# Kernel tuning notes

Hardware: AMD Instinct MI355X
Metric: run time of the kernel (lower is better)

The kernel has to match this reference:

```python
import jax, jax.numpy as jnp
import numpy as np

N, E, H, HEADS, L, B = 16000, 256000, 192, 4, 4, 8
C = H // HEADS
VN, VE, T = 32, 8, 1000


def _sin_emb(t, dim):
    half = dim // 2
    freqs = jnp.exp(-np.log(10000.0) * jnp.arange(half, dtype=jnp.float32) / half)
    ang = t.astype(jnp.float32)[:, None] * freqs[None, :]
    return jnp.concatenate([jnp.sin(ang), jnp.cos(ang)], axis=-1)


def _ln(x, g, b, eps=1e-5):
    mu = jnp.mean(x, -1, keepdims=True)
    var = jnp.mean(jnp.square(x - mu), -1, keepdims=True)
    return (x - mu) * jax.lax.rsqrt(var + eps) * g + b


def setup_inputs():
    key = jax.random.key(0)
    ks = iter(jax.random.split(key, 64))
    p = lambda shape, s=0.02: jax.random.normal(next(ks), shape, jnp.float32) * s
    inp = {}
    inp['node_emb'] = p((VN, H))
    inp['edge_emb'] = p((VE, H))
    inp['time_w1'] = p((H, H)); inp['time_b1'] = jnp.zeros((H,), jnp.float32)
    inp['time_w2'] = p((H, H)); inp['time_b2'] = jnp.zeros((H,), jnp.float32)
    inp['mask_emb'] = p((2, H))
    inp['wq'] = p((L, H, H)); inp['bq'] = jnp.zeros((L, H), jnp.float32)
    inp['wk'] = p((L, H, H)); inp['bk'] = jnp.zeros((L, H), jnp.float32)
    inp['wv'] = p((L, H, H)); inp['bv'] = jnp.zeros((L, H), jnp.float32)
    inp['we'] = p((L, H, H))
    inp['wskip'] = p((L, H, H)); inp['bskip'] = jnp.zeros((L, H), jnp.float32)
    inp['wbeta'] = p((L, 3 * H))
    inp['ln_g'] = jnp.ones((L, H), jnp.float32); inp['ln_b'] = jnp.zeros((L, H), jnp.float32)
    inp['node_out_w'] = p((H, VN)); inp['node_out_b'] = jnp.zeros((VN,), jnp.float32)
    inp['edge_w1'] = p((4 * H, H)); inp['edge_b1'] = jnp.zeros((H,), jnp.float32)
    inp['edge_w2'] = p((H, VE)); inp['edge_b2'] = jnp.zeros((VE,), jnp.float32)
    inp['node_type'] = jax.random.randint(next(ks), (N,), 0, VN)
    inp['edge_type'] = jax.random.randint(next(ks), (E,), 0, VE)
    inp['edge_index'] = jax.random.randint(next(ks), (2, E), 0, N)
    inp['edit_mask'] = jax.random.randint(next(ks), (N,), 0, 2, dtype=jnp.int32)
    inp['node_batch'] = jnp.sort(jax.random.randint(next(ks), (N,), 0, B))
    inp['t_graph'] = jax.random.randint(next(ks), (B,), 1, T)
    return inp


def reference(node_emb, edge_emb, time_w1, time_b1, time_w2, time_b2, mask_emb,
              wq, bq, wk, bk, wv, bv, we, wskip, bskip, wbeta, ln_g, ln_b,
              node_out_w, node_out_b, edge_w1, edge_b1, edge_w2, edge_b2,
              node_type, edge_type, edge_index, edit_mask, node_batch, t_graph):
    src, dst = edge_index[0], edge_index[1]
    # time embedding: sinusoidal -> Linear -> SiLU -> Linear  => [B, H]
    t_vec = jax.nn.silu(_sin_emb(t_graph, H) @ time_w1 + time_b1) @ time_w2 + time_b2
    t_node = t_vec[node_batch]              # [N, H]
    t_edge = t_vec[node_batch[src]]         # [E, H]
    x = node_emb[node_type] + t_node + mask_emb[edit_mask]
    edge_attr = edge_emb[edge_type] + t_edge
    scale = 1.0 / np.sqrt(C)
    for l in range(L):
        q = (x @ wq[l] + bq[l]).reshape(N, HEADS, C)
        k = (x @ wk[l] + bk[l]).reshape(N, HEADS, C)
        v = (x @ wv[l] + bv[l]).reshape(N, HEADS, C)
        e = (edge_attr @ we[l]).reshape(E, HEADS, C)
        kj = k[src] + e                                   # [E, heads, C]
        score = jnp.sum(q[dst] * kj, axis=-1) * scale      # [E, heads]
        m = jax.ops.segment_max(score, dst, num_segments=N)
        ex = jnp.exp(score - m[dst])
        denom = jax.ops.segment_sum(ex, dst, num_segments=N)
        alpha = ex / denom[dst]
        msg = (v[src] + e) * alpha[..., None]              # [E, heads, C]
        out = jax.ops.segment_sum(msg, dst, num_segments=N).reshape(N, H)
        xr = x @ wskip[l] + bskip[l]
        beta = jax.nn.sigmoid(jnp.concatenate([out, xr, out - xr], -1) @ wbeta[l])[:, None]
        h = beta * xr + (1.0 - beta) * out
        x = _ln(x + h, ln_g[l], ln_b[l])
    node_logits = x @ node_out_w + node_out_b
    edge_feat = jnp.concatenate([x[src], x[dst], edge_attr, t_edge], -1)  # [E, 4H]
    edge_logits = jax.nn.silu(edge_feat @ edge_w1 + edge_b1) @ edge_w2 + edge_b2
    return node_logits, edge_logits
```

## Files before the change

### kernel.cpp

```cpp
#include <hip/hip_runtime.h>
#include <hip/hip_bf16.h>
#include <math.h>

#define NN 16000
#define NPAD 16128
#define NE 256000
#define H 192
#define RP 256
#define KVR 512
#define NL 4
#define NBATCH 8
#define VEt 8
#define HH (H*H)
#define EML 16

typedef __hip_bfloat16 bf16;
typedef unsigned short u16;
typedef unsigned char u8;
typedef unsigned int u32;
typedef __attribute__((ext_vector_type(8))) short bfrag_t;
typedef __attribute__((ext_vector_type(4))) float facc_t;
typedef __attribute__((ext_vector_type(4))) float f4;
typedef __attribute__((ext_vector_type(2))) unsigned int u32x2;

__device__ __forceinline__ bf16 f2b(float v){ return __float2bfloat16(v); }
__device__ __forceinline__ int rfl(int v){ return __builtin_amdgcn_readfirstlane(v); }

__device__ __forceinline__ unsigned enc8sw(float x){
    unsigned u = __float_as_uint(x);
    unsigned s = (u >> 24) & 0x80u;
    float ax = fabsf(x);
    if(ax >= 448.f) return s | 0x7Eu;
    if(ax < 0.015625f){
        int q = (int)rintf(ax * 512.f);
        return s | (unsigned)q;
    }
    unsigned au = u & 0x7FFFFFFFu;
    unsigned lsb = (au >> 20) & 1u;
    au += 0x7FFFFu + lsb;
    unsigned E = (au >> 23) - 127u;
    unsigned M = (au >> 20) & 7u;
    if((int)E > 8) return s | 0x7Eu;
    return s | ((E + 7u) << 3) | M;
}
__device__ __forceinline__ unsigned enc8(float x){
#if __has_builtin(__builtin_amdgcn_cvt_pk_fp8_f32)
    return (u32)__builtin_amdgcn_cvt_pk_fp8_f32(x, x, 0, false) & 0xFFu;
#else
    return enc8sw(x);
#endif
}
template<int SEL>
__device__ __forceinline__ float dec8s(u32 w){
#if __has_builtin(__builtin_amdgcn_cvt_f32_fp8)
    return __builtin_amdgcn_cvt_f32_fp8((int)w, SEL);
#else
    unsigned v = (w >> (SEL*8)) & 0xFFu;
    unsigned e = (v >> 3) & 15u, m = v & 7u;
    float mag = e ? __builtin_ldexpf((float)(8u + m), (int)e - 10)
                  : __builtin_ldexpf((float)m, -9);
    return (v & 0x80u) ? -mag : mag;
#endif
}
__device__ __forceinline__ float frcp(float x){
#if __has_builtin(__builtin_amdgcn_rcpf)
    return __builtin_amdgcn_rcpf(x);
#else
    return 1.f/x;
#endif
}

__global__ void k_sentinel(float* __restrict__ out, float v){ out[0] = v; }

__global__ void k_transpose(const float* __restrict__ wq, const float* __restrict__ wk,
                            const float* __restrict__ wv, const float* __restrict__ wsk,
                            const float* __restrict__ w1, const float* __restrict__ now,
                            const float* __restrict__ ew2, u16* __restrict__ wt){
    int mat = blockIdx.x;
    if(mat < 18){
        const float* src;
        if(mat < 4)       src = wq  + (size_t)mat*HH;
        else if(mat < 8)  src = wk  + (size_t)(mat-4)*HH;
        else if(mat < 12) src = wv  + (size_t)(mat-8)*HH;
        else if(mat < 16) src = wsk + (size_t)(mat-12)*HH;
        else              src = w1  + (size_t)(mat-16)*HH;
        u16* dst = wt + (size_t)mat*HH;
        const int slice = HH/8;
        int base = blockIdx.y*slice;
        for(int i = base + threadIdx.x; i < base + slice; i += blockDim.x){
            int k = i / H, n = i % H;
            bf16 b = f2b(src[i]);
            dst[n*H + k] = *(u16*)&b;
        }
    } else if(mat == 18){
        u16* dst = wt + (size_t)18*HH;
        const int slice = (32*192)/8;
        int base = blockIdx.y*slice;
        for(int i = base + threadIdx.x; i < base + slice; i += blockDim.x){
            int k = i >> 5, n = i & 31;
            bf16 b = f2b(now[i]);
            dst[n*192 + k] = *(u16*)&b;
        }
    } else {
        u16* dst = wt + (size_t)18*HH + 32*192;
        const int slice = (16*192)/8;
        int base = blockIdx.y*slice;
        for(int i = base + threadIdx.x; i < base + slice; i += blockDim.x){
            int k = i >> 4, n = i & 15;
            float v = (n < 8) ? ew2[k*8 + n] : 0.f;
            bf16 b = f2b(v);
            dst[n*192 + k] = *(u16*)&b;
        }
    }
}

__global__ void k_tvec(const int* __restrict__ tg, const float* __restrict__ w1,
                       const float* __restrict__ b1, const float* __restrict__ w2,
                       const float* __restrict__ b2, float* __restrict__ tvec){
    int b = blockIdx.x, j = threadIdx.x;
    __shared__ float emb[H], h1[H];
    float t = (float)tg[b];
    if(j < 96){
        float fr = __expf(-logf(10000.0f) * (float)j / 96.0f);
        float ang = t * fr;
        emb[j]      = sinf(ang);
        emb[j + 96] = cosf(ang);
    }
    __syncthreads();
    float acc = b1[j];
    for(int k = 0; k < H; k++) acc += emb[k] * w1[k*H + j];
    h1[j] = acc / (1.f + __expf(-acc));
    __syncthreads();
    float acc2 = b2[j];
    for(int k = 0; k < H; k++) acc2 += h1[k] * w2[k*H + j];
    tvec[b*H + j] = acc2;
}

__global__ void k_init_x(const float* __restrict__ nemb, const float* __restrict__ memb,
                         const float* __restrict__ tvec, const int* __restrict__ ntype,
                         const int* __restrict__ emask, const int* __restrict__ nbatch,
                         float* __restrict__ x, u16* __restrict__ xb){
    int idx = blockIdx.x*blockDim.x + threadIdx.x;
    if(idx >= NN*H) return;
    int n = idx / H, c = idx % H;
    float v = nemb[(size_t)ntype[n]*H + c] + tvec[nbatch[n]*H + c]
            + memb[(size_t)emask[n]*H + c];
    x[idx] = v;
    bf16 b = f2b(v); xb[idx] = *(u16*)&b;
}

__global__ void k_zero_i(int* __restrict__ p, int n){
    int i = blockIdx.x*blockDim.x + threadIdx.x;
    if(i < n) p[i] = 0;
}
__global__ void k_count(const int* __restrict__ edst, int* __restrict__ cnt){
    int e = blockIdx.x*blockDim.x + threadIdx.x;
    if(e < NE) atomicAdd(&cnt[edst[e]], 1);
}
__global__ __launch_bounds__(1024) void k_scan(const int* __restrict__ cnt,
                                               int* __restrict__ ofs, int* __restrict__ cur){
    __shared__ int wsum[16];
    __shared__ int carry_s;
    int tid = threadIdx.x, lane = tid & 63, w = tid >> 6;
    if(tid == 0) carry_s = 0;
    __syncthreads();
    for(int base = 0; base < NN; base += 1024){
        int idx = base + tid;
        int v = (idx < NN) ? cnt[idx] : 0;
        int sc = v;
        #pragma unroll
        for(int o = 1; o < 64; o <<= 1){
            int t = __shfl_up(sc, o);
            if(lane >= o) sc += t;
        }
        if(lane == 63) wsum[w] = sc;
        __syncthreads();
        if(w == 0){
            int ws = (lane < 16) ? wsum[lane] : 0;
            #pragma unroll
            for(int o = 1; o < 16; o <<= 1){
                int t = __shfl_up(ws, o);
                if(lane >= o) ws += t;
            }
            if(lane < 16) wsum[lane] = ws;
        }
        __syncthreads();
        int wbase = (w > 0) ? wsum[w-1] : 0;
        int c = carry_s;
        int excl = c + wbase + sc - v;
        if(idx < NN){ ofs[idx] = excl; cur[idx] = excl; }
        __syncthreads();
        if(tid == 0) carry_s = c + wsum[15];
        __syncthreads();
    }
    if(threadIdx.x == 0) ofs[NN] = carry_s;
}
__global__ void k_scatter(const int* __restrict__ esrc, const int* __restrict__ edst,
                          const int* __restrict__ etype, const int* __restrict__ nbatch,
                          int* __restrict__ cur, int2* __restrict__ spair){
    int e = blockIdx.x*blockDim.x + threadIdx.x;
    if(e >= NE) return;
    int s = esrc[e], d = edst[e];
    int pos = atomicAdd(&cur[d], 1);
    int2 se; se.x = s*KVR; se.y = (nbatch[s]*VEt + etype[e])*KVR;
    spair[pos] = se;
}

__global__ void k_tabs(const float* __restrict__ eemb, const float* __restrict__ tvec,
                       const float* __restrict__ we,
                       const float* __restrict__ w1, const float* __restrict__ b1,
                       u16* __restrict__ etab, u16* __restrict__ ctab){
    int blk = blockIdx.x;
    int c = threadIdx.x;
    __shared__ float a[H];
    if(blk < NL*64){
        int l = blk >> 6, idx = blk & 63, b = idx >> 3, et = idx & 7;
        a[c] = eemb[et*H + c] + tvec[b*H + c];
        __syncthreads();
        float acc = 0.f;
        const float* w = we + (size_t)l*HH;
        for(int k = 0; k < H; k++) acc += a[k] * w[k*H + c];
        bf16 bv = f2b(acc);
        etab[(size_t)blk*256 + (c/3)*4 + (c%3)] = *(u16*)&bv;
    } else {
        int idx = blk - NL*64, b = idx >> 3, et = idx & 7;
        a[c] = eemb[et*H + c] + tvec[b*H + c];
        __syncthreads();
        float acc = b1[c];
        for(int k = 0; k < H; k++){
            acc += a[k]          * w1[(size_t)(2*H + k)*H + c];
            acc += tvec[b*H + k] * w1[(size_t)(3*H + k)*H + c];
        }
        bf16 bv = f2b(acc);
        ctab[(size_t)idx*256 + (c/3)*4 + (c%3)] = *(u16*)&bv;
    }
}

struct GemmP {
    const u16* wt[4];
    const float* bias[4];
    void* out[4];
    int obf[4];
};
__global__ __launch_bounds__(256) void k_gemm(const u16* __restrict__ A, GemmP P){
    int oi = blockIdx.y / 3, nt = blockIdx.y % 3;
    const u16* Wt = P.wt[oi];
    const float* bias = P.bias[oi];
    int wave = rfl(threadIdx.x >> 6), lane = threadIdx.x & 63;
    int quad = lane >> 4, l16 = lane & 15;
    int m0 = blockIdx.x*256 + wave*64;
    int n0 = nt*64;
    facc_t acc[4][4];
    #pragma unroll
    for(int i = 0; i < 4; i++)
        #pragma unroll
        for(int j = 0; j < 4; j++){ acc[i][j][0]=0.f; acc[i][j][1]=0.f; acc[i][j][2]=0.f; acc[i][j][3]=0.f; }
    #pragma unroll
    for(int kc = 0; kc < 6; kc++){
        int kb = kc*32 + quad*8;
        bfrag_t af[4], bg[4];
        #pragma unroll
        for(int i = 0; i < 4; i++) af[i] = *(const bfrag_t*)(A  + (size_t)(m0 + i*16 + l16)*H + kb);
        #pragma unroll
        for(int j = 0; j < 4; j++) bg[j] = *(const bfrag_t*)(Wt + (size_t)(n0 + j*16 + l16)*H + kb);
        #pragma unroll
        for(int i = 0; i < 4; i++)
            #pragma unroll
            for(int j = 0; j < 4; j++)
                acc[i][j] = __builtin_amdgcn_mfma_f32_16x16x32_bf16(af[i], bg[j], acc[i][j], 0, 0, 0);
    }
    float bv[4];
    #pragma unroll
    for(int j = 0; j < 4; j++) bv[j] = bias ? bias[n0 + j*16 + l16] : 0.f;
    int mode = P.obf[oi];
    if(mode != 0){
        u8* out = (u8*)P.out[oi];
        int rstride = (mode == 2) ? RP : KVR;
        int mult    = (mode == 2) ? 4  : 8;
        int koff    = (mode == 4) ? 4  : 0;
        int byteoff[4];
        #pragma unroll
        for(int j = 0; j < 4; j++){
            int c = n0 + j*16 + l16;
            byteoff[j] = (c/3)*mult + (c%3) + koff;
        }
        #pragma unroll
        for(int i = 0; i < 4; i++){
            int rb = m0 + i*16 + quad*4;
            #pragma unroll
            for(int r = 0; r < 4; r++){
                int row = rb + r;
                if(row < NN){
                    #pragma unroll
                    for(int j = 0; j < 4; j++)
                        out[(size_t)row*rstride + byteoff[j]] = (u8)enc8(acc[i][j][r] + bv[j]);
                }
            }
        }
    } else {
        float* out = (float*)P.out[oi];
        #pragma unroll
        for(int i = 0; i < 4; i++){
            int rb = m0 + i*16 + quad*4;
            #pragma unroll
            for(int r = 0; r < 4; r++){
                int row = rb + r;
                if(row < NN){
                    #pragma unroll
                    for(int j = 0; j < 4; j++)
                        out[(size_t)row*H + n0 + j*16 + l16] = acc[i][j][r] + bv[j];
                }
            }
        }
    }
}

__global__ __launch_bounds__(256) void k_attn(
    const float* __restrict__ Q, const u8* __restrict__ KVb,
    const float* __restrict__ XR,
    const u16* __restrict__ etab, const int* __restrict__ ofs,
    const int2* __restrict__ spair,
    const float* __restrict__ wb, const float* __restrict__ lng, const float* __restrict__ lnb,
    float* __restrict__ x, u16* __restrict__ xb)
{
    int wv = rfl(threadIdx.x >> 6);
    int n = blockIdx.x*4 + wv;
    int lane = threadIdx.x & 63;
    int lane8 = lane*8;
    int ch = lane*3;
    size_t base = (size_t)n*H + ch;
    const float scale = 0.14433756729740646f;
    float q0 = Q[base], q1 = Q[base+1], q2 = Q[base+2];
    int p0 = ofs[n], p1 = ofs[n+1];
    float lac[4]  = {0.f,0.f,0.f,0.f};
    float ac0[4]  = {0.f,0.f,0.f,0.f};
    float ac1[4]  = {0.f,0.f,0.f,0.f};
    float ac2[4]  = {0.f,0.f,0.f,0.f};
    const u8* etb = (const u8*)etab;
    int p = p0;
    u32x2 kvc[4], ewc[4];
    bool have = (p + 3 < p1);
    if(have){
        #pragma unroll
        for(int t = 0; t < 4; t++){
            int2 se = spair[p+t];
            kvc[t] = *(const u32x2*)(KVb + se.x + lane8);
            ewc[t] = *(const u32x2*)(etb + se.y + lane8);
        }
    }
    while(have){
        int pn = p + 4;
        bool more = (pn + 3 < p1);
        u32x2 kvn[4], ewn[4];
        if(more){
            #pragma unroll
            for(int t = 0; t < 4; t++){
                int2 se = spair[pn+t];
                kvn[t] = *(const u32x2*)(KVb + se.x + lane8);
                ewn[t] = *(const u32x2*)(etb + se.y + lane8);
            }
        }
        float e0[4], e1[4], e2[4], tt[4];
        #pragma unroll
        for(int t = 0; t < 4; t++){
            e0[t] = __uint_as_float(ewc[t].x << 16);
            e1[t] = __uint_as_float(ewc[t].x & 0xffff0000u);
            e2[t] = __uint_as_float(ewc[t].y << 16);
            tt[t] = q0*(dec8s<0>(kvc[t].x)+e0[t]) + q1*(dec8s<1>(kvc[t].x)+e1[t])
                  + q2*(dec8s<2>(kvc[t].x)+e2[t]);
        }
        #pragma unroll
        for(int o = 1; o <= 8; o <<= 1){
            #pragma unroll
            for(int t = 0; t < 4; t++) tt[t] += __shfl_xor(tt[t], o);
        }
        #pragma unroll
        for(int t = 0; t < 4; t++){
            float sc = fminf(fmaxf(tt[t]*scale, -60.f), 60.f);
            float pw = __expf(sc);
            lac[t] += pw;
            ac0[t] += pw*(dec8s<0>(kvc[t].y)+e0[t]);
            ac1[t] += pw*(dec8s<1>(kvc[t].y)+e1[t]);
            ac2[t] += pw*(dec8s<2>(kvc[t].y)+e2[t]);
        }
        if(more){
            #pragma unroll
            for(int t = 0; t < 4; t++){ kvc[t] = kvn[t]; ewc[t] = ewn[t]; }
        }
        p = pn;
        have = more;
    }
    for(; p < p1; p++){
        int soA = spair[p].x, eoA = spair[p].y;
        u32x2 kvA = *(const u32x2*)(KVb + soA + lane8);
        u32x2 ewA = *(const u32x2*)(etb + eoA + lane8);
        float e0A = __uint_as_float(ewA.x << 16);
        float e1A = __uint_as_float(ewA.x & 0xffff0000u);
        float e2A = __uint_as_float(ewA.y << 16);
        float tA = q0*(dec8s<0>(kvA.x)+e0A) + q1*(dec8s<1>(kvA.x)+e1A) + q2*(dec8s<2>(kvA.x)+e2A);
        tA += __shfl_xor(tA,1); tA += __shfl_xor(tA,2); tA += __shfl_xor(tA,4); tA += __shfl_xor(tA,8);
        float sc = fminf(fmaxf(tA*scale, -60.f), 60.f);
        float pw = __expf(sc);
        lac[0] += pw;
        ac0[0] += pw*(dec8s<0>(kvA.y)+e0A);
        ac1[0] += pw*(dec8s<1>(kvA.y)+e1A);
        ac2[0] += pw*(dec8s<2>(kvA.y)+e2A);
    }
    float l  = (lac[0]+lac[1]) + (lac[2]+lac[3]);
    float a0 = (ac0[0]+ac0[1]) + (ac0[2]+ac0[3]);
    float a1 = (ac1[0]+ac1[1]) + (ac1[2]+ac1[3]);
    float a2 = (ac2[0]+ac2[1]) + (ac2[2]+ac2[3]);
    float inv = (p1 > p0) ? 1.f/l : 0.f;
    float o0 = a0*inv, o1 = a1*inv, o2 = a2*inv;
    float xr0 = XR[base], xr1 = XR[base+1], xr2 = XR[base+2];
    float sd = o0*wb[ch]  + o1*wb[ch+1]  + o2*wb[ch+2]
             + xr0*wb[H+ch] + xr1*wb[H+ch+1] + xr2*wb[H+ch+2]
             + (o0-xr0)*wb[2*H+ch] + (o1-xr1)*wb[2*H+ch+1] + (o2-xr2)*wb[2*H+ch+2];
    sd += __shfl_xor(sd,1); sd += __shfl_xor(sd,2); sd += __shfl_xor(sd,4);
    sd += __shfl_xor(sd,8); sd += __shfl_xor(sd,16); sd += __shfl_xor(sd,32);
    float beta = 1.f/(1.f + __expf(-sd));
    float h0 = beta*xr0 + (1.f-beta)*o0;
    float h1 = beta*xr1 + (1.f-beta)*o1;
    float h2 = beta*xr2 + (1.f-beta)*o2;
    float y0 = x[base] + h0, y1 = x[base+1] + h1, y2 = x[base+2] + h2;
    float s3 = y0 + y1 + y2;
    float q3 = y0*y0 + y1*y1 + y2*y2;
    #pragma unroll
    for(int o = 1; o <= 32; o <<= 1){
        s3 += __shfl_xor(s3, o);
        q3 += __shfl_xor(q3, o);
    }
    float mean = s3 * (1.f/H);
    float var = fmaxf(q3*(1.f/H) - mean*mean, 0.f);
    float rs = rsqrtf(var + 1e-5f);
    float d0 = y0-mean, d1 = y1-mean, d2 = y2-mean;
    float z0 = d0*rs*lng[ch]   + lnb[ch];
    float z1 = d1*rs*lng[ch+1] + lnb[ch+1];
    float z2 = d2*rs*lng[ch+2] + lnb[ch+2];
    x[base] = z0; x[base+1] = z1; x[base+2] = z2;
    bf16 t0 = f2b(z0), t1 = f2b(z1), t2 = f2b(z2);
    xb[base] = *(u16*)&t0; xb[base+1] = *(u16*)&t1; xb[base+2] = *(u16*)&t2;
}

__global__ __launch_bounds__(256) void k_nodeout(const u16* __restrict__ A, const u16* __restrict__ Wt,
                                                 const float* __restrict__ b, float* __restrict__ out){
    int wave = rfl(threadIdx.x >> 6), lane = threadIdx.x & 63;
    int quad = lane >> 4, l16 = lane & 15;
    int m0 = blockIdx.x*256 + wave*64;
    facc_t acc[4][2];
    #pragma unroll
    for(int i = 0; i < 4; i++)
        #pragma unroll
        for(int j = 0; j < 2; j++){ acc[i][j][0]=0.f; acc[i][j][1]=0.f; acc[i][j][2]=0.f; acc[i][j][3]=0.f; }
    #pragma unroll
    for(int kc = 0; kc < 6; kc++){
        int kb = kc*32 + quad*8;
        bfrag_t af[4], bg[2];
        #pragma unroll
        for(int i = 0; i < 4; i++) af[i] = *(const bfrag_t*)(A  + (size_t)(m0 + i*16 + l16)*H + kb);
        #pragma unroll
        for(int j = 0; j < 2; j++) bg[j] = *(const bfrag_t*)(Wt + (size_t)(j*16 + l16)*H + kb);
        #pragma unroll
        for(int i = 0; i < 4; i++)
            #pragma unroll
            for(int j = 0; j < 2; j++)
                acc[i][j] = __builtin_amdgcn_mfma_f32_16x16x32_bf16(af[i], bg[j], acc[i][j], 0, 0, 0);
    }
    float bv[2];
    #pragma unroll
    for(int j = 0; j < 2; j++) bv[j] = b[j*16 + l16];
    #pragma unroll
    for(int i = 0; i < 4; i++){
        int rb = m0 + i*16 + quad*4;
        #pragma unroll
        for(int r = 0; r < 4; r++){
            int row = rb + r;
            if(row < NN){
                #pragma unroll
                for(int j = 0; j < 2; j++)
                    out[(size_t)row*32 + j*16 + l16] = acc[i][j][r] + bv[j];
            }
        }
    }
}

__global__ __launch_bounds__(256) void k_edgemlp(
    const int* __restrict__ esrc, const int* __restrict__ edst, const int* __restrict__ etype,
    const int* __restrict__ nb,
    const u8* __restrict__ xs1, const u8* __restrict__ xd1, const u16* __restrict__ ctab,
    const u16* __restrict__ w2t, const float* __restrict__ b2p, float* __restrict__ out)
{
    __shared__ u16 hbuf[4][16][200];
    int wave = rfl(threadIdx.x >> 6);
    int lane = threadIdx.x & 63;
    int lane8 = lane*8;
    int l16 = lane & 15, quad = lane >> 4;
    int wid = blockIdx.x*4 + wave;
    int e0 = wid*EML;
    const u8* ctb = (const u8*)ctab;
    bfrag_t bg[6];
    #pragma unroll
    for(int kc = 0; kc < 6; kc++)
        bg[kc] = *(const bfrag_t*)(w2t + (size_t)l16*192 + kc*32 + quad*8);
    for(int eb = 0; eb < EML; eb += 2){
        int eX = e0 + eb, eY = e0 + eb + 1;
        int sX = esrc[eX], dX = edst[eX];
        int sY = esrc[eY], dY = edst[eY];
        int coX = (nb[sX]*VEt + etype[eX])*KVR;
        int coY = (nb[sY]*VEt + etype[eY])*KVR;
        u32 awX = *(const u32*)(xs1 + (size_t)sX*RP + lane*4);
        u32 awY = *(const u32*)(xs1 + (size_t)sY*RP + lane*4);
        u32 bwX = *(const u32*)(xd1 + (size_t)dX*RP + lane*4);
        u32 bwY = *(const u32*)(xd1 + (size_t)dY*RP + lane*4);
        u32x2 cwX = *(const u32x2*)(ctb + coX + lane8);
        u32x2 cwY = *(const u32x2*)(ctb + coY + lane8);
        float cfX0 = __uint_as_float(cwX.x << 16);
        float cfX1 = __uint_as_float(cwX.x & 0xffff0000u);
        float cfX2 = __uint_as_float(cwX.y << 16);
        float cfY0 = __uint_as_float(cwY.x << 16);
        float cfY1 = __uint_as_float(cwY.x & 0xffff0000u);
        float cfY2 = __uint_as_float(cwY.y << 16);
        float hX0, hX1, hX2, hY0, hY1, hY2;
        { float v = dec8s<0>(awX)+dec8s<0>(bwX)+cfX0; hX0 = v*frcp(1.f+__expf(-v)); }
        { float v = dec8s<1>(awX)+dec8s<1>(bwX)+cfX1; hX1 = v*frcp(1.f+__expf(-v)); }
        { float v = dec8s<2>(awX)+dec8s<2>(bwX)+cfX2; hX2 = v*frcp(1.f+__expf(-v)); }
        { float v = dec8s<0>(awY)+dec8s<0>(bwY)+cfY0; hY0 = v*frcp(1.f+__expf(-v)); }
        { float v = dec8s<1>(awY)+dec8s<1>(bwY)+cfY1; hY1 = v*frcp(1.f+__expf(-v)); }
        { float v = dec8s<2>(awY)+dec8s<2>(bwY)+cfY2; hY2 = v*frcp(1.f+__expf(-v)); }
        u16* rowX = &hbuf[wave][eb][0];
        u16* rowY = &hbuf[wave][eb+1][0];
        bf16 x0 = f2b(hX0), x1 = f2b(hX1), x2 = f2b(hX2);
        bf16 y0 = f2b(hY0), y1 = f2b(hY1), y2 = f2b(hY2);
        rowX[lane*3+0] = *(u16*)&x0; rowX[lane*3+1] = *(u16*)&x1; rowX[lane*3+2] = *(u16*)&x2;
        rowY[lane*3+0] = *(u16*)&y0; rowY[lane*3+1] = *(u16*)&y1; rowY[lane*3+2] = *(u16*)&y2;
    }
    __syncthreads();
    facc_t acc;
    acc[0]=0.f; acc[1]=0.f; acc[2]=0.f; acc[3]=0.f;
    #pragma unroll
    for(int kc = 0; kc < 6; kc++){
        bfrag_t af = *(const bfrag_t*)&hbuf[wave][l16][kc*32 + quad*8];
        acc = __builtin_amdgcn_mfma_f32_16x16x32_bf16(af, bg[kc], acc, 0, 0, 0);
    }
    if(l16 < 8){
        float bo = b2p[l16];
        #pragma unroll
        for(int r = 0; r < 4; r++){
            int e = e0 + quad*4 + r;
            out[(size_t)e*8 + l16] = acc[r] + bo;
        }
    }
}

extern "C" void kernel_launch(void* const* d_in, const int* in_sizes, int n_in,
                              void* d_out, int out_size, void* d_ws, size_t ws_size,
                              hipStream_t stream)
{
    {
        int bad = -1;
        if(n_in != 31) bad = 100;
        else {
            const int chk_idx[9] = {0, 7, 16, 21, 23, 26, 27, 29, 30};
            const int chk_sz [9] = {32*H, NL*HH, NL*3*H, 4*HH, H*8, NE, 2*NE, NN, NBATCH};
            for(int i = 0; i < 9; i++) if(in_sizes[chk_idx[i]] != chk_sz[i]){ bad = chk_idx[i]; break; }
        }
        if(bad >= 0){ k_sentinel<<<1,1,0,stream>>>((float*)d_out, 20000.f + 256.f*bad); return; }
        if(out_size != NN*32 + NE*8){ k_sentinel<<<1,1,0,stream>>>((float*)d_out, 30000.f); return; }
    }

    const float* node_emb = (const float*)d_in[0];
    const float* edge_emb = (const float*)d_in[1];
    const float* time_w1  = (const float*)d_in[2];
    const float* time_b1  = (const float*)d_in[3];
    const float* time_w2  = (const float*)d_in[4];
    const float* time_b2  = (const float*)d_in[5];
    const float* mask_emb = (const float*)d_in[6];
    const float* wq       = (const float*)d_in[7];
    const float* bq       = (const float*)d_in[8];
    const float* wk       = (const float*)d_in[9];
    const float* bk       = (const float*)d_in[10];
    const float* wv       = (const float*)d_in[11];
    const float* bv       = (const float*)d_in[12];
    const float* we       = (const float*)d_in[13];
    const float* wskip    = (const float*)d_in[14];
    const float* bskip    = (const float*)d_in[15];
    const float* wbeta    = (const float*)d_in[16];
    const float* ln_g     = (const float*)d_in[17];
    const float* ln_b     = (const float*)d_in[18];
    const float* now      = (const float*)d_in[19];
    const float* nob      = (const float*)d_in[20];
    const float* ew1      = (const float*)d_in[21];
    const float* eb1      = (const float*)d_in[22];
    const float* ew2      = (const float*)d_in[23];
    const float* eb2      = (const float*)d_in[24];
    const int* node_type  = (const int*)d_in[25];
    const int* edge_type  = (const int*)d_in[26];
    const int* edge_index = (const int*)d_in[27];
    const int* edit_mask  = (const int*)d_in[28];
    const int* node_batch = (const int*)d_in[29];
    const int* t_graph    = (const int*)d_in[30];
    const int* esrc = edge_index;
    const int* edst = edge_index + NE;

    char* wsb = (char*)d_ws;
    size_t off = 0;
    auto take = [&](size_t bytes) -> char* {
        char* r = wsb + off;
        off += (bytes + 255) & ~(size_t)255;
        return r;
    };
    float* tvec = (float*)take((size_t)NBATCH*H*4);
    float* x    = (float*)take((size_t)NN*H*4);
    u16*   xb   = (u16*)  take((size_t)NPAD*H*2);
    float* Q    = (float*)take((size_t)NN*H*4);
    u8*    KVb  = (u8*)   take((size_t)NN*KVR);
    float* XR   = (float*)take((size_t)NN*H*4);
    u8*    xs1  = (u8*)   take((size_t)NN*RP);
    u8*    xd1  = (u8*)   take((size_t)NN*RP);
    u16*   etab = (u16*)  take((size_t)NL*64*KVR);
    u16*   ctab = (u16*)  take((size_t)64*KVR);
    u16*   wt   = (u16*)  take((size_t)(18*HH + 32*192 + 16*192)*2);
    int* cnt    = (int*)  take((size_t)(NN+1)*4);
    int* offa   = (int*)  take((size_t)(NN+1)*4);
    int* cur    = (int*)  take((size_t)(NN+1)*4);
    int2* spair = (int2*) take((size_t)NE*8);

    if(ws_size < off){
        k_sentinel<<<1,1,0,stream>>>((float*)d_out, 10000.f + (float)(ws_size >> 20));
        return;
    }

    u16* w32t = wt + (size_t)18*HH;
    u16* w2t  = w32t + 32*192;

    k_transpose<<<dim3(20, 8), 256, 0, stream>>>(wq, wk, wv, wskip, ew1, now, ew2, wt);
    k_tvec<<<NBATCH, H, 0, stream>>>(t_graph, time_w1, time_b1, time_w2, time_b2, tvec);
    k_init_x<<<(NN*H + 255)/256, 256, 0, stream>>>(node_emb, mask_emb, tvec, node_type,
                                                   edit_mask, node_batch, x, xb);
    k_zero_i<<<(NN + 255)/256, 256, 0, stream>>>(cnt, NN);
    k_count<<<NE/256, 256, 0, stream>>>(edst, cnt);
    k_scan<<<1, 1024, 0, stream>>>(cnt, offa, cur);
    k_scatter<<<NE/256, 256, 0, stream>>>(esrc, edst, edge_type, node_batch, cur, spair);
    k_tabs<<<NL*64 + 64, H, 0, stream>>>(edge_emb, tvec, we, ew1, eb1, etab, ctab);

    for(int l = 0; l < NL; l++){
        GemmP P;
        P.wt[0] = wt + (size_t)(0  + l)*HH;  P.bias[0] = bq   + (size_t)l*H;  P.out[0] = Q;   P.obf[0] = 0;
        P.wt[1] = wt + (size_t)(4  + l)*HH;  P.bias[1] = bk   + (size_t)l*H;  P.out[1] = KVb; P.obf[1] = 3;
        P.wt[2] = wt + (size_t)(8  + l)*HH;  P.bias[2] = bv   + (size_t)l*H;  P.out[2] = KVb; P.obf[2] = 4;
        P.wt[3] = wt + (size_t)(12 + l)*HH;  P.bias[3] = bskip+ (size_t)l*H;  P.out[3] = XR;  P.obf[3] = 0;
        k_gemm<<<dim3(63, 12), 256, 0, stream>>>(xb, P);
        k_attn<<<NN/4, 256, 0, stream>>>(Q, KVb, XR, etab + (size_t)l*64*256, offa, spair,
                                         wbeta + (size_t)l*3*H, ln_g + (size_t)l*H,
                                         ln_b + (size_t)l*H, x, xb);
    }
    {
        GemmP P;
        P.wt[0] = wt + (size_t)16*HH; P.bias[0] = nullptr; P.out[0] = xs1; P.obf[0] = 2;
        P.wt[1] = wt + (size_t)17*HH; P.bias[1] = nullptr; P.out[1] = xd1; P.obf[1] = 2;
        P.wt[2] = P.wt[0]; P.bias[2] = nullptr; P.out[2] = xs1; P.obf[2] = 2;
        P.wt[3] = P.wt[0]; P.bias[3] = nullptr; P.out[3] = xs1; P.obf[3] = 2;
        k_gemm<<<dim3(63, 6), 256, 0, stream>>>(xb, P);
    }
    k_nodeout<<<63, 256, 0, stream>>>(xb, w32t, nob, (float*)d_out);
    k_edgemlp<<<NE/(4*EML), 256, 0, stream>>>(esrc, edst, edge_type, node_batch, xs1, xd1, ctab,
                                              w2t, eb2, (float*)d_out + (size_t)NN*32);
}
```

Baseline: 502.3 us.

## Fuse setup kernels, store Q as packed bf16, precompute edge indices, packed fp8 decode

Merges the weight transpose, time embedding and counter zeroing into one launch, and merges x init, degree counting and edge tables into another. This cuts the number of small kernel launches. Q is now written by the GEMM as bf16 in the padded attention layout, which roughly halves its read traffic in the attention kernel but lowers its precision. The scatter pass precomputes per-edge src, dst and table offsets so the edge MLP needs one int4 load instead of several dependent gathers. fp8 decode uses the packed two-value conversion where it is available.

```diff
diff --git a/kernel.cpp b/kernel.cpp
--- a/kernel.cpp
+++ b/kernel.cpp
@@ -22,6 +22,7 @@
 typedef __attribute__((ext_vector_type(4))) float facc_t;
 typedef __attribute__((ext_vector_type(4))) float f4;
 typedef __attribute__((ext_vector_type(2))) unsigned int u32x2;
+typedef __attribute__((ext_vector_type(2))) float f2v;
 
 __device__ __forceinline__ bf16 f2b(float v){ return __float2bfloat16(v); }
 __device__ __forceinline__ int rfl(int v){ return __builtin_amdgcn_readfirstlane(v); }
@@ -62,6 +63,13 @@
     return (v & 0x80u) ? -mag : mag;
 #endif
 }
+__device__ __forceinline__ f2v dec8pk01(u32 w){
+#if __has_builtin(__builtin_amdgcn_cvt_pk_f32_fp8)
+    return __builtin_amdgcn_cvt_pk_f32_fp8((int)w, false);
+#else
+    f2v r; r.x = dec8s<0>(w); r.y = dec8s<1>(w); return r;
+#endif
+}
 __device__ __forceinline__ float frcp(float x){
 #if __has_builtin(__builtin_amdgcn_rcpf)
     return __builtin_amdgcn_rcpf(x);
@@ -72,91 +80,131 @@
 
 __global__ void k_sentinel(float* __restrict__ out, float v){ out[0] = v; }
 
-__global__ void k_transpose(const float* __restrict__ wq, const float* __restrict__ wk,
-                            const float* __restrict__ wv, const float* __restrict__ wsk,
-                            const float* __restrict__ w1, const float* __restrict__ now,
-                            const float* __restrict__ ew2, u16* __restrict__ wt){
-    int mat = blockIdx.x;
-    if(mat < 18){
-        const float* src;
-        if(mat < 4)       src = wq  + (size_t)mat*HH;
-        else if(mat < 8)  src = wk  + (size_t)(mat-4)*HH;
-        else if(mat < 12) src = wv  + (size_t)(mat-8)*HH;
-        else if(mat < 16) src = wsk + (size_t)(mat-12)*HH;
-        else              src = w1  + (size_t)(mat-16)*HH;
-        u16* dst = wt + (size_t)mat*HH;
-        const int slice = HH/8;
-        int base = blockIdx.y*slice;
-        for(int i = base + threadIdx.x; i < base + slice; i += blockDim.x){
-            int k = i / H, n = i % H;
-            bf16 b = f2b(src[i]);
-            dst[n*H + k] = *(u16*)&b;
-        }
-    } else if(mat == 18){
-        u16* dst = wt + (size_t)18*HH;
-        const int slice = (32*192)/8;
-        int base = blockIdx.y*slice;
-        for(int i = base + threadIdx.x; i < base + slice; i += blockDim.x){
-            int k = i >> 5, n = i & 31;
-            bf16 b = f2b(now[i]);
-            dst[n*192 + k] = *(u16*)&b;
+__global__ void k_prep0(const float* __restrict__ wq, const float* __restrict__ wk,
+                        const float* __restrict__ wv, const float* __restrict__ wsk,
+                        const float* __restrict__ w1, const float* __restrict__ now,
+                        const float* __restrict__ ew2, u16* __restrict__ wt,
+                        const int* __restrict__ tg, const float* __restrict__ tw1,
+                        const float* __restrict__ tb1, const float* __restrict__ tw2,
+                        const float* __restrict__ tb2, float* __restrict__ tvec,
+                        int* __restrict__ cnt){
+    int blk = blockIdx.x;
+    if(blk < 160){
+        int mat = blk >> 3, ys = blk & 7;
+        if(mat < 18){
+            const float* src;
+            if(mat < 4)       src = wq  + (size_t)mat*HH;
+            else if(mat < 8)  src = wk  + (size_t)(mat-4)*HH;
+            else if(mat < 12) src = wv  + (size_t)(mat-8)*HH;
+            else if(mat < 16) src = wsk + (size_t)(mat-12)*HH;
+            else              src = w1  + (size_t)(mat-16)*HH;
+            u16* dst = wt + (size_t)mat*HH;
+            const int slice = HH/8;
+            int base = ys*slice;
+            for(int i = base + threadIdx.x; i < base + slice; i += blockDim.x){
+                int k = i / H, n = i % H;
+                bf16 b = f2b(src[i]);
+                dst[n*H + k] = *(u16*)&b;
+            }
+        } else if(mat == 18){
+            u16* dst = wt + (size_t)18*HH;
+            const int slice = (32*192)/8;
+            int base = ys*slice;
+            for(int i = base + threadIdx.x; i < base + slice; i += blockDim.x){
+                int k = i >> 5, n = i & 31;
+                bf16 b = f2b(now[i]);
+                dst[n*192 + k] = *(u16*)&b;
+            }
+        } else {
+            u16* dst = wt + (size_t)18*HH + 32*192;
+            const int slice = (16*192)/8;
+            int base = ys*slice;
+            for(int i = base + threadIdx.x; i < base + slice; i += blockDim.x){
+                int k = i >> 4, n = i & 15;
+                float v = (n < 8) ? ew2[k*8 + n] : 0.f;
+                bf16 b = f2b(v);
+                dst[n*192 + k] = *(u16*)&b;
+            }
+        }
+    } else if(blk < 168){
+        int b = blk - 160, j = threadIdx.x;
+        __shared__ float emb[H], h1[H];
+        float t = (float)tg[b];
+        if(j < 96){
+            float fr = __expf(-logf(10000.0f) * (float)j / 96.0f);
+            float ang = t * fr;
+            emb[j]      = sinf(ang);
+            emb[j + 96] = cosf(ang);
+        }
+        __syncthreads();
+        if(j < H){
+            float acc = tb1[j];
+            for(int k = 0; k < H; k++) acc += emb[k] * tw1[k*H + j];
+            h1[j] = acc / (1.f + __expf(-acc));
+        }
+        __syncthreads();
+        if(j < H){
+            float acc2 = tb2[j];
+            for(int k = 0; k < H; k++) acc2 += h1[k] * tw2[k*H + j];
+            tvec[b*H + j] = acc2;
         }
     } else {
-        u16* dst = wt + (size_t)18*HH + 32*192;
-        const int slice = (16*192)/8;
-        int base = blockIdx.y*slice;
-        for(int i = base + threadIdx.x; i < base + slice; i += blockDim.x){
-            int k = i >> 4, n = i & 15;
-            float v = (n < 8) ? ew2[k*8 + n] : 0.f;
-            bf16 b = f2b(v);
-            dst[n*192 + k] = *(u16*)&b;
-        }
-    }
-}
-
-__global__ void k_tvec(const int* __restrict__ tg, const float* __restrict__ w1,
-                       const float* __restrict__ b1, const float* __restrict__ w2,
-                       const float* __restrict__ b2, float* __restrict__ tvec){
-    int b = blockIdx.x, j = threadIdx.x;
-    __shared__ float emb[H], h1[H];
-    float t = (float)tg[b];
-    if(j < 96){
-        float fr = __expf(-logf(10000.0f) * (float)j / 96.0f);
-        float ang = t * fr;
-        emb[j]      = sinf(ang);
-        emb[j + 96] = cosf(ang);
-    }
-    __syncthreads();
-    float acc = b1[j];
-    for(int k = 0; k < H; k++) acc += emb[k] * w1[k*H + j];
-    h1[j] = acc / (1.f + __expf(-acc));
-    __syncthreads();
-    float acc2 = b2[j];
-    for(int k = 0; k < H; k++) acc2 += h1[k] * w2[k*H + j];
-    tvec[b*H + j] = acc2;
-}
-
-__global__ void k_init_x(const float* __restrict__ nemb, const float* __restrict__ memb,
-                         const float* __restrict__ tvec, const int* __restrict__ ntype,
-                         const int* __restrict__ emask, const int* __restrict__ nbatch,
-                         float* __restrict__ x, u16* __restrict__ xb){
-    int idx = blockIdx.x*blockDim.x + threadIdx.x;
-    if(idx >= NN*H) return;
-    int n = idx / H, c = idx % H;
-    float v = nemb[(size_t)ntype[n]*H + c] + tvec[nbatch[n]*H + c]
-            + memb[(size_t)emask[n]*H + c];
-    x[idx] = v;
-    bf16 b = f2b(v); xb[idx] = *(u16*)&b;
-}
-
-__global__ void k_zero_i(int* __restrict__ p, int n){
-    int i = blockIdx.x*blockDim.x + threadIdx.x;
-    if(i < n) p[i] = 0;
-}
-__global__ void k_count(const int* __restrict__ edst, int* __restrict__ cnt){
-    int e = blockIdx.x*blockDim.x + threadIdx.x;
-    if(e < NE) atomicAdd(&cnt[edst[e]], 1);
-}
+        int i = (blk - 168)*256 + threadIdx.x;
+        if(i < NN+1) cnt[i] = 0;
+    }
+}
+
+__global__ void k_prep1(const float* __restrict__ nemb, const float* __restrict__ memb,
+                        const float* __restrict__ tvec, const int* __restrict__ ntype,
+                        const int* __restrict__ emask, const int* __restrict__ nbatch,
+                        float* __restrict__ x, u16* __restrict__ xb,
+                        const int* __restrict__ edst, int* __restrict__ cnt,
+                        const float* __restrict__ eemb, const float* __restrict__ we,
+                        const float* __restrict__ w1, const float* __restrict__ b1,
+                        u16* __restrict__ etab, u16* __restrict__ ctab){
+    int blk = blockIdx.x;
+    if(blk < 12000){
+        int idx = blk*256 + threadIdx.x;
+        int n = idx / H, c = idx % H;
+        float v = nemb[(size_t)ntype[n]*H + c] + tvec[nbatch[n]*H + c]
+                + memb[(size_t)emask[n]*H + c];
+        x[idx] = v;
+        bf16 b = f2b(v); xb[idx] = *(u16*)&b;
+    } else if(blk < 13000){
+        int e = (blk - 12000)*256 + threadIdx.x;
+        atomicAdd(&cnt[edst[e]], 1);
+    } else {
+        int blk2 = blk - 13000;
+        int c = threadIdx.x;
+        __shared__ float a[H];
+        if(blk2 < NL*64){
+            int l = blk2 >> 6, idx = blk2 & 63, b = idx >> 3, et = idx & 7;
+            if(c < H) a[c] = eemb[et*H + c] + tvec[b*H + c];
+            __syncthreads();
+            if(c < H){
+                float acc = 0.f;
+                const float* w = we + (size_t)l*HH;
+                for(int k = 0; k < H; k++) acc += a[k] * w[k*H + c];
+                bf16 bv = f2b(acc);
+                etab[(size_t)blk2*256 + (c/3)*4 + (c%3)] = *(u16*)&bv;
+            }
+        } else {
+            int idx = blk2 - NL*64, b = idx >> 3, et = idx & 7;
+            if(c < H) a[c] = eemb[et*H + c] + tvec[b*H + c];
+            __syncthreads();
+            if(c < H){
+                float acc = b1[c];
+                for(int k = 0; k < H; k++){
+                    acc += a[k]          * w1[(size_t)(2*H + k)*H + c];
+                    acc += tvec[b*H + k] * w1[(size_t)(3*H + k)*H + c];
+                }
+                bf16 bv = f2b(acc);
+                ctab[(size_t)idx*256 + (c/3)*4 + (c%3)] = *(u16*)&bv;
+            }
+        }
+    }
+}
+
 __global__ __launch_bounds__(1024) void k_scan(const int* __restrict__ cnt,
                                                int* __restrict__ ofs, int* __restrict__ cur){
     __shared__ int wsum[16];
@@ -197,43 +245,15 @@
 }
 __global__ void k_scatter(const int* __restrict__ esrc, const int* __restrict__ edst,
                           const int* __restrict__ etype, const int* __restrict__ nbatch,
-                          int* __restrict__ cur, int2* __restrict__ spair){
+                          int* __restrict__ cur, int2* __restrict__ spair, int4* __restrict__ eprep){
     int e = blockIdx.x*blockDim.x + threadIdx.x;
     if(e >= NE) return;
     int s = esrc[e], d = edst[e];
+    int ct = (nbatch[s]*VEt + etype[e])*KVR;
     int pos = atomicAdd(&cur[d], 1);
-    int2 se; se.x = s*KVR; se.y = (nbatch[s]*VEt + etype[e])*KVR;
+    int2 se; se.x = s*KVR; se.y = ct;
     spair[pos] = se;
-}
-
-__global__ void k_tabs(const float* __restrict__ eemb, const float* __restrict__ tvec,
-                       const float* __restrict__ we,
-                       const float* __restrict__ w1, const float* __restrict__ b1,
-                       u16* __restrict__ etab, u16* __restrict__ ctab){
-    int blk = blockIdx.x;
-    int c = threadIdx.x;
-    __shared__ float a[H];
-    if(blk < NL*64){
-        int l = blk >> 6, idx = blk & 63, b = idx >> 3, et = idx & 7;
-        a[c] = eemb[et*H + c] + tvec[b*H + c];
-        __syncthreads();
-        float acc = 0.f;
-        const float* w = we + (size_t)l*HH;
-        for(int k = 0; k < H; k++) acc += a[k] * w[k*H + c];
-        bf16 bv = f2b(acc);
-        etab[(size_t)blk*256 + (c/3)*4 + (c%3)] = *(u16*)&bv;
-    } else {
-        int idx = blk - NL*64, b = idx >> 3, et = idx & 7;
-        a[c] = eemb[et*H + c] + tvec[b*H + c];
-        __syncthreads();
-        float acc = b1[c];
-        for(int k = 0; k < H; k++){
-            acc += a[k]          * w1[(size_t)(2*H + k)*H + c];
-            acc += tvec[b*H + k] * w1[(size_t)(3*H + k)*H + c];
-        }
-        bf16 bv = f2b(acc);
-        ctab[(size_t)idx*256 + (c/3)*4 + (c%3)] = *(u16*)&bv;
-    }
+    eprep[e] = make_int4(s*RP, d*RP, ct, 0);
 }
 
 struct GemmP {
@@ -273,7 +293,30 @@
     #pragma unroll
     for(int j = 0; j < 4; j++) bv[j] = bias ? bias[n0 + j*16 + l16] : 0.f;
     int mode = P.obf[oi];
-    if(mode != 0){
+    if(mode == 5){
+        u16* outp = (u16*)P.out[oi];
+        int hoff[4];
+        #pragma unroll
+        for(int j = 0; j < 4; j++){
+            int c = n0 + j*16 + l16;
+            hoff[j] = (c/3)*4 + (c%3);
+        }
+        #pragma unroll
+        for(int i = 0; i < 4; i++){
+            int rb = m0 + i*16 + quad*4;
+            #pragma unroll
+            for(int r = 0; r < 4; r++){
+                int row = rb + r;
+                if(row < NN){
+                    #pragma unroll
+                    for(int j = 0; j < 4; j++){
+                        bf16 b = f2b(acc[i][j][r] + bv[j]);
+                        outp[(size_t)row*256 + hoff[j]] = *(u16*)&b;
+                    }
+                }
+            }
+        }
+    } else if(mode != 0){
         u8* out = (u8*)P.out[oi];
         int rstride = (mode == 2) ? RP : KVR;
         int mult    = (mode == 2) ? 4  : 8;
@@ -316,7 +359,7 @@
 }
 
 __global__ __launch_bounds__(256) void k_attn(
-    const float* __restrict__ Q, const u8* __restrict__ KVb,
+    const u8* __restrict__ Qb, const u8* __restrict__ KVb,
     const float* __restrict__ XR,
     const u16* __restrict__ etab, const int* __restrict__ ofs,
     const int2* __restrict__ spair,
@@ -330,7 +373,10 @@
     int ch = lane*3;
     size_t base = (size_t)n*H + ch;
     const float scale = 0.14433756729740646f;
-    float q0 = Q[base], q1 = Q[base+1], q2 = Q[base+2];
+    u32x2 qw = *(const u32x2*)(Qb + (size_t)n*512 + lane8);
+    float q0 = __uint_as_float(qw.x << 16);
+    float q1 = __uint_as_float(qw.x & 0xffff0000u);
+    float q2 = __uint_as_float(qw.y << 16);
     int p0 = ofs[n], p1 = ofs[n+1];
     float lac[4]  = {0.f,0.f,0.f,0.f};
     float ac0[4]  = {0.f,0.f,0.f,0.f};
@@ -366,8 +412,9 @@
             e0[t] = __uint_as_float(ewc[t].x << 16);
             e1[t] = __uint_as_float(ewc[t].x & 0xffff0000u);
             e2[t] = __uint_as_float(ewc[t].y << 16);
-            tt[t] = q0*(dec8s<0>(kvc[t].x)+e0[t]) + q1*(dec8s<1>(kvc[t].x)+e1[t])
-                  + q2*(dec8s<2>(kvc[t].x)+e2[t]);
+            f2v k01 = dec8pk01(kvc[t].x);
+            float k2 = dec8s<2>(kvc[t].x);
+            tt[t] = q0*(k01.x+e0[t]) + q1*(k01.y+e1[t]) + q2*(k2+e2[t]);
         }
         #pragma unroll
         for(int o = 1; o <= 8; o <<= 1){
@@ -378,10 +425,12 @@
         for(int t = 0; t < 4; t++){
             float sc = fminf(fmaxf(tt[t]*scale, -60.f), 60.f);
             float pw = __expf(sc);
+            f2v v01 = dec8pk01(kvc[t].y);
+            float v2 = dec8s<2>(kvc[t].y);
             lac[t] += pw;
-            ac0[t] += pw*(dec8s<0>(kvc[t].y)+e0[t]);
-            ac1[t] += pw*(dec8s<1>(kvc[t].y)+e1[t]);
-            ac2[t] += pw*(dec8s<2>(kvc[t].y)+e2[t]);
+            ac0[t] += pw*(v01.x+e0[t]);
+            ac1[t] += pw*(v01.y+e1[t]);
+            ac2[t] += pw*(v2+e2[t]);
         }
         if(more){
             #pragma unroll
@@ -397,14 +446,18 @@
         float e0A = __uint_as_float(ewA.x << 16);
         float e1A = __uint_as_float(ewA.x & 0xffff0000u);
         float e2A = __uint_as_float(ewA.y << 16);
-        float tA = q0*(dec8s<0>(kvA.x)+e0A) + q1*(dec8s<1>(kvA.x)+e1A) + q2*(dec8s<2>(kvA.x)+e2A);
+        f2v k01 = dec8pk01(kvA.x);
+        float k2 = dec8s<2>(kvA.x);
+        float tA = q0*(k01.x+e0A) + q1*(k01.y+e1A) + q2*(k2+e2A);
         tA += __shfl_xor(tA,1); tA += __shfl_xor(tA,2); tA += __shfl_xor(tA,4); tA += __shfl_xor(tA,8);
         float sc = fminf(fmaxf(tA*scale, -60.f), 60.f);
         float pw = __expf(sc);
+        f2v v01 = dec8pk01(kvA.y);
+        float v2 = dec8s<2>(kvA.y);
         lac[0] += pw;
-        ac0[0] += pw*(dec8s<0>(kvA.y)+e0A);
-        ac1[0] += pw*(dec8s<1>(kvA.y)+e1A);
-        ac2[0] += pw*(dec8s<2>(kvA.y)+e2A);
+        ac0[0] += pw*(v01.x+e0A);
+        ac1[0] += pw*(v01.y+e1A);
+        ac2[0] += pw*(v2+e2A);
     }
     float l  = (lac[0]+lac[1]) + (lac[2]+lac[3]);
     float a0 = (ac0[0]+ac0[1]) + (ac0[2]+ac0[3]);
@@ -485,8 +538,7 @@
 }
 
 __global__ __launch_bounds__(256) void k_edgemlp(
-    const int* __restrict__ esrc, const int* __restrict__ edst, const int* __restrict__ etype,
-    const int* __restrict__ nb,
+    const int4* __restrict__ eprep,
     const u8* __restrict__ xs1, const u8* __restrict__ xd1, const u16* __restrict__ ctab,
     const u16* __restrict__ w2t, const float* __restrict__ b2p, float* __restrict__ out)
 {
@@ -503,30 +555,31 @@
     for(int kc = 0; kc < 6; kc++)
         bg[kc] = *(const bfrag_t*)(w2t + (size_t)l16*192 + kc*32 + quad*8);
     for(int eb = 0; eb < EML; eb += 2){
-        int eX = e0 + eb, eY = e0 + eb + 1;
-        int sX = esrc[eX], dX = edst[eX];
-        int sY = esrc[eY], dY = edst[eY];
-        int coX = (nb[sX]*VEt + etype[eX])*KVR;
-        int coY = (nb[sY]*VEt + etype[eY])*KVR;
-        u32 awX = *(const u32*)(xs1 + (size_t)sX*RP + lane*4);
-        u32 awY = *(const u32*)(xs1 + (size_t)sY*RP + lane*4);
-        u32 bwX = *(const u32*)(xd1 + (size_t)dX*RP + lane*4);
-        u32 bwY = *(const u32*)(xd1 + (size_t)dY*RP + lane*4);
-        u32x2 cwX = *(const u32x2*)(ctb + coX + lane8);
-        u32x2 cwY = *(const u32x2*)(ctb + coY + lane8);
+        int4 epX = eprep[e0 + eb];
+        int4 epY = eprep[e0 + eb + 1];
+        u32 awX = *(const u32*)(xs1 + epX.x + lane*4);
+        u32 awY = *(const u32*)(xs1 + epY.x + lane*4);
+        u32 bwX = *(const u32*)(xd1 + epX.y + lane*4);
+        u32 bwY = *(const u32*)(xd1 + epY.y + lane*4);
+        u32x2 cwX = *(const u32x2*)(ctb + epX.z + lane8);
+        u32x2 cwY = *(const u32x2*)(ctb + epY.z + lane8);
         float cfX0 = __uint_as_float(cwX.x << 16);
         float cfX1 = __uint_as_float(cwX.x & 0xffff0000u);
         float cfX2 = __uint_as_float(cwX.y << 16);
         float cfY0 = __uint_as_float(cwY.x << 16);
         float cfY1 = __uint_as_float(cwY.x & 0xffff0000u);
         float cfY2 = __uint_as_float(cwY.y << 16);
+        f2v aX = dec8pk01(awX), bX = dec8pk01(bwX);
+        f2v aY = dec8pk01(awY), bY = dec8pk01(bwY);
+        float aX2 = dec8s<2>(awX), bX2 = dec8s<2>(bwX);
+        float aY2 = dec8s<2>(awY), bY2 = dec8s<2>(bwY);
         float hX0, hX1, hX2, hY0, hY1, hY2;
-        { float v = dec8s<0>(awX)+dec8s<0>(bwX)+cfX0; hX0 = v*frcp(1.f+__expf(-v)); }
-        { float v = dec8s<1>(awX)+dec8s<1>(bwX)+cfX1; hX1 = v*frcp(1.f+__expf(-v)); }
-        { float v = dec8s<2>(awX)+dec8s<2>(bwX)+cfX2; hX2 = v*frcp(1.f+__expf(-v)); }
-        { float v = dec8s<0>(awY)+dec8s<0>(bwY)+cfY0; hY0 = v*frcp(1.f+__expf(-v)); }
-        { float v = dec8s<1>(awY)+dec8s<1>(bwY)+cfY1; hY1 = v*frcp(1.f+__expf(-v)); }
-        { float v = dec8s<2>(awY)+dec8s<2>(bwY)+cfY2; hY2 = v*frcp(1.f+__expf(-v)); }
+        { float v = aX.x+bX.x+cfX0; hX0 = v*frcp(1.f+__expf(-v)); }
+        { float v = aX.y+bX.y+cfX1; hX1 = v*frcp(1.f+__expf(-v)); }
+        { float v = aX2 +bX2 +cfX2; hX2 = v*frcp(1.f+__expf(-v)); }
+        { float v = aY.x+bY.x+cfY0; hY0 = v*frcp(1.f+__expf(-v)); }
+        { float v = aY.y+bY.y+cfY1; hY1 = v*frcp(1.f+__expf(-v)); }
+        { float v = aY2 +bY2 +cfY2; hY2 = v*frcp(1.f+__expf(-v)); }
         u16* rowX = &hbuf[wave][eb][0];
         u16* rowY = &hbuf[wave][eb+1][0];
         bf16 x0 = f2b(hX0), x1 = f2b(hX1), x2 = f2b(hX2);
@@ -612,7 +665,7 @@
     float* tvec = (float*)take((size_t)NBATCH*H*4);
     float* x    = (float*)take((size_t)NN*H*4);
     u16*   xb   = (u16*)  take((size_t)NPAD*H*2);
-    float* Q    = (float*)take((size_t)NN*H*4);
+    u8*    Qb   = (u8*)   take((size_t)NN*512);
     u8*    KVb  = (u8*)   take((size_t)NN*KVR);
     float* XR   = (float*)take((size_t)NN*H*4);
     u8*    xs1  = (u8*)   take((size_t)NN*RP);
@@ -624,6 +677,7 @@
     int* offa   = (int*)  take((size_t)(NN+1)*4);
     int* cur    = (int*)  take((size_t)(NN+1)*4);
     int2* spair = (int2*) take((size_t)NE*8);
+    int4* eprep = (int4*) take((size_t)NE*16);
 
     if(ws_size < off){
         k_sentinel<<<1,1,0,stream>>>((float*)d_out, 10000.f + (float)(ws_size >> 20));
@@ -633,24 +687,21 @@
     u16* w32t = wt + (size_t)18*HH;
     u16* w2t  = w32t + 32*192;
 
-    k_transpose<<<dim3(20, 8), 256, 0, stream>>>(wq, wk, wv, wskip, ew1, now, ew2, wt);
-    k_tvec<<<NBATCH, H, 0, stream>>>(t_graph, time_w1, time_b1, time_w2, time_b2, tvec);
-    k_init_x<<<(NN*H + 255)/256, 256, 0, stream>>>(node_emb, mask_emb, tvec, node_type,
-                                                   edit_mask, node_batch, x, xb);
-    k_zero_i<<<(NN + 255)/256, 256, 0, stream>>>(cnt, NN);
-    k_count<<<NE/256, 256, 0, stream>>>(edst, cnt);
+    k_prep0<<<231, 256, 0, stream>>>(wq, wk, wv, wskip, ew1, now, ew2, wt,
+                                     t_graph, time_w1, time_b1, time_w2, time_b2, tvec, cnt);
+    k_prep1<<<13320, 256, 0, stream>>>(node_emb, mask_emb, tvec, node_type, edit_mask, node_batch,
+                                       x, xb, edst, cnt, edge_emb, we, ew1, eb1, etab, ctab);
     k_scan<<<1, 1024, 0, stream>>>(cnt, offa, cur);
-    k_scatter<<<NE/256, 256, 0, stream>>>(esrc, edst, edge_type, node_batch, cur, spair);
-    k_tabs<<<NL*64 + 64, H, 0, stream>>>(edge_emb, tvec, we, ew1, eb1, etab, ctab);
+    k_scatter<<<NE/256, 256, 0, stream>>>(esrc, edst, edge_type, node_batch, cur, spair, eprep);
 
     for(int l = 0; l < NL; l++){
         GemmP P;
-        P.wt[0] = wt + (size_t)(0  + l)*HH;  P.bias[0] = bq   + (size_t)l*H;  P.out[0] = Q;   P.obf[0] = 0;
+        P.wt[0] = wt + (size_t)(0  + l)*HH;  P.bias[0] = bq   + (size_t)l*H;  P.out[0] = Qb;  P.obf[0] = 5;
         P.wt[1] = wt + (size_t)(4  + l)*HH;  P.bias[1] = bk   + (size_t)l*H;  P.out[1] = KVb; P.obf[1] = 3;
         P.wt[2] = wt + (size_t)(8  + l)*HH;  P.bias[2] = bv   + (size_t)l*H;  P.out[2] = KVb; P.obf[2] = 4;
         P.wt[3] = wt + (size_t)(12 + l)*HH;  P.bias[3] = bskip+ (size_t)l*H;  P.out[3] = XR;  P.obf[3] = 0;
         k_gemm<<<dim3(63, 12), 256, 0, stream>>>(xb, P);
-        k_attn<<<NN/4, 256, 0, stream>>>(Q, KVb, XR, etab + (size_t)l*64*256, offa, spair,
+        k_attn<<<NN/4, 256, 0, stream>>>(Qb, KVb, XR, etab + (size_t)l*64*256, offa, spair,
                                          wbeta + (size_t)l*3*H, ln_g + (size_t)l*H,
                                          ln_b + (size_t)l*H, x, xb);
     }
@@ -663,6 +714,6 @@
         k_gemm<<<dim3(63, 6), 256, 0, stream>>>(xb, P);
     }
     k_nodeout<<<63, 256, 0, stream>>>(xb, w32t, nob, (float*)d_out);
-    k_edgemlp<<<NE/(4*EML), 256, 0, stream>>>(esrc, edst, edge_type, node_batch, xs1, xd1, ctab,
+    k_edgemlp<<<NE/(4*EML), 256, 0, stream>>>(eprep, xs1, xd1, ctab,
                                               w2t, eb2, (float*)d_out + (size_t)NN*32);
 }
```

New measurement: 459.3 us (median of 2 runs). -8.6%, faster.
